# Kernel tuning notes

Measured on AMD Instinct MI355X. Metric: run time of the kernel, lower is better.

## Reference

```python
import jax, jax.numpy as jnp
import numpy as np

B, T, NE, NH, HD = 4, 1024, 768, 12, 64
CURV = 0.0
EPS = 1e-6
LN_EPS = 1e-5
ROPE_BASE = 10000.0


def project(x, k):
    # Lift Euclidean vector onto Lorentz hyperboloid with curvature K = exp(k):
    # time coord t = sqrt(K + ||x||^2) so that <lx, lx>_L = -K.
    K = jnp.exp(k)
    t = jnp.sqrt(K + jnp.sum(x * x, axis=-1, keepdims=True))
    return jnp.concatenate([t, x], axis=-1)


def lorentz_distance(lq, lk, k):
    # lq, lk: (B, H, T, D+1); k: (1, H, 1, 1) log-curvature.
    # d = sqrt(K) * arccosh(clamp(-<q,k>_L / K, 1+eps))
    K = jnp.exp(k)
    inner = (jnp.einsum('bhid,bhjd->bhij', lq[..., 1:], lk[..., 1:])
             - jnp.einsum('bhi,bhj->bhij', lq[..., 0], lk[..., 0]))
    c = jnp.clip(-inner / K, 1.0 + EPS, None)
    return jnp.sqrt(K) * jnp.arccosh(c)


def lorentz_norm(x):
    # sqrt(|<x,x>_L|) with <x,x>_L = -x0^2 + ||xs||^2  (keepdim)
    inner = -x[..., 0:1] ** 2 + jnp.sum(x[..., 1:] ** 2, axis=-1, keepdims=True)
    return jnp.sqrt(jnp.clip(-inner, EPS, None))


def rotary_tables():
    inv_freq = 1.0 / (ROPE_BASE ** (np.arange(0, HD, 2, dtype=np.float32) / HD))
    t = np.arange(T, dtype=np.float32)
    freqs = np.outer(t, inv_freq)  # (T, HD/2)
    cos = jnp.asarray(np.cos(freqs))[None, :, None, :]  # (1,T,1,HD/2)
    sin = jnp.asarray(np.sin(freqs))[None, :, None, :]
    return cos, sin


def apply_rotary(x, cos, sin):
    # x: (B, T, H, HD)
    x1, x2 = x[..., : HD // 2], x[..., HD // 2:]
    return jnp.concatenate([x1 * cos + x2 * sin, -x1 * sin + x2 * cos], axis=-1)


def layernorm(y, g, b):
    m = jnp.mean(y, axis=-1, keepdims=True)
    v = jnp.mean((y - m) ** 2, axis=-1, keepdims=True)
    return (y - m) / jnp.sqrt(v + LN_EPS) * g + b


def setup_inputs() -> dict:
    key = jax.random.key(0)
    ks = jax.random.split(key, 8)
    s = 0.02
    return {
        'x': jax.random.normal(ks[0], (B, T, NE), dtype=jnp.float32),
        'block_curvature': jnp.asarray(CURV, dtype=jnp.float32),
        'mlp_curvature': jnp.asarray(CURV, dtype=jnp.float32),
        'attn_curvatures': jnp.ones((1, NH, 1, 1), dtype=jnp.float32) * CURV,
        'qkv_w': jax.random.normal(ks[1], (3 * NE, NE + 1), dtype=jnp.float32) * s,
        'attn_proj_w': jax.random.normal(ks[2], (NE, (HD + 1) * NH), dtype=jnp.float32) * s,
        'attn_proj_b': jnp.zeros((NE,), dtype=jnp.float32),
        'mlp_expand_w': jax.random.normal(ks[3], (4 * NE + 3, NE + 1), dtype=jnp.float32) * s,
        'mlp_expand_b': jnp.zeros((4 * NE + 3,), dtype=jnp.float32),
        'mlp_shrink_w': jax.random.normal(ks[4], (NE, 4 * (NE + 1)), dtype=jnp.float32) * s,
        'mlp_shrink_b': jnp.zeros((NE,), dtype=jnp.float32),
        'ln_g': jnp.ones((NE,), dtype=jnp.float32),
        'ln_b': jnp.zeros((NE,), dtype=jnp.float32),
    }


def reference(x, block_curvature, mlp_curvature, attn_curvatures, qkv_w,
              attn_proj_w, attn_proj_b, mlp_expand_w, mlp_expand_b,
              mlp_shrink_w, mlp_shrink_b, ln_g, ln_b):
    cos, sin = rotary_tables()
    causal_bias = jnp.where(
        jnp.triu(jnp.ones((T, T), dtype=bool), k=1), -jnp.inf, 0.0).astype(jnp.float32)

    def block_norm(lx):
        return project(layernorm(lx[..., 1:], ln_g, ln_b), block_curvature)

    def attn(lx):
        qkv = lx @ qkv_w.T  # (B, T, 3*NE)
        q, k, v = jnp.split(qkv, 3, axis=-1)
        q = apply_rotary(q.reshape(B, T, NH, HD), cos, sin)
        k = apply_rotary(k.reshape(B, T, NH, HD), cos, sin)
        v = v.reshape(B, T, NH, HD)
        lq = project(q.transpose(0, 2, 1, 3), attn_curvatures)  # (B,H,T,HD+1)
        lk = project(k.transpose(0, 2, 1, 3), attn_curvatures)
        lv = project(v.transpose(0, 2, 1, 3), attn_curvatures)
        dis = lorentz_distance(lq, lk, attn_curvatures)  # (B,H,T,T)
        aw = jax.nn.softmax(-dis + causal_bias, axis=-1)
        a = jnp.einsum('bhij,bhjd->bhid', aw, lv)  # (B,H,T,HD+1)
        a = a * jnp.sqrt(jnp.exp(attn_curvatures)) / lorentz_norm(a)
        a = a.transpose(0, 2, 1, 3).reshape(B, T, NH * (HD + 1))
        a = a @ attn_proj_w.T + attn_proj_b
        return project(a, block_curvature)

    def mlp(lx):
        h = lx @ mlp_expand_w.T + mlp_expand_b  # (B,T,4*NE+3)
        h = project(h, mlp_curvature)[..., 1:]  # drop time coord back to 4*NE+3
        h = jax.nn.gelu(h, approximate=False)
        h = project(h, mlp_curvature)  # (B,T,4*(NE+1))
        h = h @ mlp_shrink_w.T + mlp_shrink_b
        return project(h, block_curvature)

    def skip(lx, f_lx):
        return project(lx[..., 1:] + f_lx[..., 1:], block_curvature)

    lx = project(x, block_curvature)  # (B,T,NE+1)
    lx = skip(lx, attn(block_norm(lx)))
    lx = skip(lx, mlp(block_norm(lx)))
    return lx
```

## Files before the change

### kernel.cpp

```cpp
#include <hip/hip_runtime.h>
#include <cmath>

typedef unsigned short ushort_t;
typedef __attribute__((ext_vector_type(8))) short short8;
typedef __attribute__((ext_vector_type(4))) float floatx4;

#define NH    12
#define T     1024
#define ROWS  4096
#define NE    768
#define KPA   832
#define KPB   3136
#define NEXP  3200
#define HEXP  3075
#define NSPLIT 3

__device__ __forceinline__ ushort_t f2bf(float f) {
  union { float f; unsigned u; } v; v.f = f;
  unsigned r = v.u + 0x7fffu + ((v.u >> 16) & 1u);
  return (ushort_t)(r >> 16);
}
__device__ __forceinline__ ushort_t f2bf_trunc(float f) {
  union { float f; unsigned u; } v; v.f = f;
  return (ushort_t)(v.u >> 16);
}
__device__ __forceinline__ float bf2f(ushort_t b) {
  union { unsigned u; float f; } v; v.u = ((unsigned)b) << 16;
  return v.f;
}
__device__ __forceinline__ float blk_reduce_sum(float v, float* sm) {
  #pragma unroll
  for (int o = 32; o > 0; o >>= 1) v += __shfl_xor(v, o, 64);
  int lane = threadIdx.x & 63, w = threadIdx.x >> 6;
  __syncthreads();
  if (lane == 0) sm[w] = v;
  __syncthreads();
  return sm[0] + sm[1] + sm[2] + sm[3];
}
__device__ __forceinline__ float red16_sum(float v) {
  #pragma unroll
  for (int o = 1; o < 16; o <<= 1) v += __shfl_xor(v, o, 64);
  return v;
}

#define NB_A 7488
#define NB_B 2496
#define NB_C 10400
#define NB_D 9408
#define NB_E 16
__device__ __forceinline__ void cvt_elem(ushort_t* __restrict__ dst,
                                         const float* __restrict__ src,
                                         int idx, int srcRows, int srcK, int dstK) {
  int r = idx / dstK, c = idx - r * dstK;
  dst[idx] = (r < srcRows && c < srcK) ? f2bf(src[(size_t)r * srcK + c]) : (ushort_t)0;
}
__global__ __launch_bounds__(256) void prep_kernel(
    ushort_t* __restrict__ qkv_wb, const float* __restrict__ qkvw,
    ushort_t* __restrict__ proj_wb, const float* __restrict__ projw,
    ushort_t* __restrict__ exp_wb, const float* __restrict__ expw,
    ushort_t* __restrict__ shr_wb, const float* __restrict__ shrw,
    ushort_t* __restrict__ aout_bf,
    const float* __restrict__ xin, const float* __restrict__ g,
    const float* __restrict__ bb, const float* __restrict__ curv,
    ushort_t* __restrict__ lnp) {
  __shared__ float sm[4];
  int blk = blockIdx.x;
  int tid = threadIdx.x;
  if (blk < NB_A) {
    cvt_elem(qkv_wb, qkvw, blk * 256 + tid, 2304, 769, KPA);
  } else if (blk < NB_A + NB_B) {
    cvt_elem(proj_wb, projw, (blk - NB_A) * 256 + tid, 768, 780, KPA);
  } else if (blk < NB_A + NB_B + NB_C) {
    cvt_elem(exp_wb, expw, (blk - NB_A - NB_B) * 256 + tid, HEXP, 769, KPA);
  } else if (blk < NB_A + NB_B + NB_C + NB_D) {
    cvt_elem(shr_wb, shrw, (blk - NB_A - NB_B - NB_C) * 256 + tid, 768, 3076, KPB);
  } else if (blk < NB_A + NB_B + NB_C + NB_D + NB_E) {
    int r = (blk - NB_A - NB_B - NB_C - NB_D) * 256 + tid;
    ushort_t* p = aout_bf + (size_t)r * KPA + 780;
    #pragma unroll
    for (int j = 0; j < KPA - 780; ++j) p[j] = 0;
  } else {
    const int row = blk - (NB_A + NB_B + NB_C + NB_D + NB_E);
    const float* xr = xin + (size_t)row * NE;
    float xv[3];
    float s = 0.f, ss = 0.f;
    #pragma unroll
    for (int i = 0; i < 3; ++i) {
      xv[i] = xr[tid + 256 * i];
      s += xv[i]; ss += xv[i] * xv[i];
    }
    s = blk_reduce_sum(s, sm);
    ss = blk_reduce_sum(ss, sm);
    float mean = s * (1.f / 768.f);
    float var = ss * (1.f / 768.f) - mean * mean;
    float rstd = rsqrtf(var + 1e-5f);
    float yv[3]; float ys = 0.f;
    #pragma unroll
    for (int i = 0; i < 3; ++i) {
      int c = tid + 256 * i;
      yv[i] = (xv[i] - mean) * rstd * g[c] + bb[c];
      ys += yv[i] * yv[i];
    }
    ys = blk_reduce_sum(ys, sm);
    float tc = sqrtf(expf(curv[0]) + ys);
    ushort_t* orow = lnp + (size_t)row * KPA;
    #pragma unroll
    for (int i = 0; i < 3; ++i) orow[1 + tid + 256 * i] = f2bf(yv[i]);
    if (tid == 0) orow[0] = f2bf(tc);
    if (tid < KPA - 769) orow[769 + tid] = 0;
  }
}

__global__ __launch_bounds__(256) void gemm_bf16(
    const ushort_t* __restrict__ A, int lda,
    const ushort_t* __restrict__ W, int ldw,
    void* __restrict__ Cout, int ldc,
    int nkTot, int cpt,
    const float* __restrict__ bias, int biasN,
    const float* __restrict__ res, int ldres,
    int outMode, void* __restrict__ Cp) {
  __shared__ ushort_t As[128 * 64];
  __shared__ ushort_t Bs[128 * 64];
  const int tid = threadIdx.x;
  const int w = tid >> 6, lane = tid & 63;

  int bx = blockIdx.x, by = blockIdx.y;
  {
    const int gx = gridDim.x, gy = gridDim.y;
    const int nwg = gx * gy;
    if ((nwg & 7) == 0) {
      int lin = by * gx + bx;
      int swz = (lin & 7) * (nwg >> 3) + (lin >> 3);
      bx = swz % gx;
      by = swz / gx;
    }
  }
  const int rowBase = by << 7;
  const int colBase = bx << 7;
  const int wm = (w & 1) * 64, wn = (w >> 1) * 64;
  const int lm = lane & 15, quad = lane >> 4;
  const int p0 = quad ^ (lm & 7);

  floatx4 acc[4][4];
  #pragma unroll
  for (int i = 0; i < 4; ++i)
    #pragma unroll
    for (int j = 0; j < 4; ++j) {
      floatx4 z = {0.f, 0.f, 0.f, 0.f};
      acc[i][j] = z;
    }

  const int kt0 = (int)blockIdx.z * cpt;
  const int kt1 = min(nkTot, kt0 + cpt);
  for (int kt = kt0; kt < kt1; ++kt) {
    __syncthreads();
    #pragma unroll
    for (int j = 0; j < 4; ++j) {
      int ci = j * 256 + tid;
      int r = ci >> 3;
      int g = (ci & 7) ^ (r & 7);
      const ushort_t* ga = A + (size_t)(rowBase + r) * lda + kt * 64 + g * 8;
      const ushort_t* gb = W + (size_t)(colBase + r) * ldw + kt * 64 + g * 8;
      __builtin_amdgcn_global_load_lds(
          (const __attribute__((address_space(1))) void*)ga,
          (__attribute__((address_space(3))) void*)&As[(j * 256 + w * 64) * 8],
          16, 0, 0);
      __builtin_amdgcn_global_load_lds(
          (const __attribute__((address_space(1))) void*)gb,
          (__attribute__((address_space(3))) void*)&Bs[(j * 256 + w * 64) * 8],
          16, 0, 0);
    }
    __syncthreads();

    #pragma unroll
    for (int s = 0; s < 2; ++s) {
      const int ps = s ? (p0 ^ 4) : p0;
      short8 af[4], bfr[4];
      #pragma unroll
      for (int i = 0; i < 4; ++i) {
        af[i]  = *(const short8*)&As[(wm + i * 16 + lm) * 64 + ps * 8];
        bfr[i] = *(const short8*)&Bs[(wn + i * 16 + lm) * 64 + ps * 8];
      }
      #pragma unroll
      for (int i = 0; i < 4; ++i)
        #pragma unroll
        for (int jn = 0; jn < 4; ++jn)
          acc[i][jn] = __builtin_amdgcn_mfma_f32_16x16x32_bf16(
              af[i], bfr[jn], acc[i][jn], 0, 0, 0);
    }
  }

  if (gridDim.z > 1) {
    ushort_t* dst = (ushort_t*)Cp + (size_t)blockIdx.z * ROWS * ldc;
    #pragma unroll
    for (int i = 0; i < 4; ++i)
      #pragma unroll
      for (int jn = 0; jn < 4; ++jn) {
        const int col = colBase + wn + jn * 16 + lm;
        #pragma unroll
        for (int rg = 0; rg < 4; ++rg) {
          const int row = rowBase + wm + i * 16 + quad * 4 + rg;
          dst[(size_t)row * ldc + col] = f2bf(acc[i][jn][rg]);
        }
      }
  } else if (outMode == 1) {
    ushort_t* C = (ushort_t*)Cout;
    #pragma unroll
    for (int i = 0; i < 4; ++i)
      #pragma unroll
      for (int jn = 0; jn < 4; ++jn) {
        const int col = colBase + wn + jn * 16 + lm;
        const float bv = bias ? ((col < biasN) ? bias[col] : 0.f) : 0.f;
        #pragma unroll
        for (int rg = 0; rg < 4; ++rg) {
          const int row = rowBase + wm + i * 16 + quad * 4 + rg;
          C[(size_t)row * ldc + col] = f2bf(acc[i][jn][rg] + bv);
        }
      }
  } else {
    float* C = (float*)Cout;
    #pragma unroll
    for (int i = 0; i < 4; ++i)
      #pragma unroll
      for (int jn = 0; jn < 4; ++jn) {
        const int col = colBase + wn + jn * 16 + lm;
        const float bv = bias ? ((col < biasN) ? bias[col] : 0.f) : 0.f;
        #pragma unroll
        for (int rg = 0; rg < 4; ++rg) {
          const int row = rowBase + wm + i * 16 + quad * 4 + rg;
          float o = acc[i][jn][rg] + bv;
          if (res) o += res[(size_t)row * ldres + col];
          C[(size_t)row * ldc + col] = o;
        }
      }
  }
}

__global__ __launch_bounds__(256) void rope_project(
    const ushort_t* __restrict__ qkvp, const float* __restrict__ ac,
    ushort_t* __restrict__ qb, ushort_t* __restrict__ kb, ushort_t* __restrict__ vtb,
    float* __restrict__ q0, float* __restrict__ k0, float* __restrict__ v0) {
  int gid = blockIdx.x * 4 + (threadIdx.x >> 6);
  int lane = threadIdx.x & 63;
  int h = gid % NH;
  int bt = gid / NH;
  int t = bt & (T - 1);
  int b = bt >> 10;
  size_t base = (size_t)bt * 2304 + h * 64;
  const ushort_t* p1 = qkvp + (size_t)ROWS * 2304;
  float qv = bf2f(qkvp[base + lane])        + bf2f(p1[base + lane]);
  float kv = bf2f(qkvp[base + 768 + lane])  + bf2f(p1[base + 768 + lane]);
  float vv = bf2f(qkvp[base + 1536 + lane]) + bf2f(p1[base + 1536 + lane]);
  int f = lane & 31;
  float ang = (float)t * __builtin_amdgcn_exp2f(-(float)f * 0.4152410118661534f);
  float sn, cs;
  sincosf(ang, &sn, &cs);
  float qp = __shfl(qv, lane ^ 32, 64);
  float kp = __shfl(kv, lane ^ 32, 64);
  float qr = (lane < 32) ? (qv * cs + qp * sn) : (-qp * sn + qv * cs);
  float kr = (lane < 32) ? (kv * cs + kp * sn) : (-kp * sn + kv * cs);
  float Kh = expf(ac[h]);
  float sq = qr * qr, sk = kr * kr, sv = vv * vv;
  #pragma unroll
  for (int o = 32; o > 0; o >>= 1) {
    sq += __shfl_xor(sq, o, 64);
    sk += __shfl_xor(sk, o, 64);
    sv += __shfl_xor(sv, o, 64);
  }
  size_t idx = ((size_t)(b * NH + h) * T + t);
  qb[idx * 64 + lane] = f2bf(qr);
  kb[idx * 64 + lane] = f2bf(kr);
  vtb[(size_t)(b * NH + h) * (64 * T) + (size_t)lane * T + t] = f2bf(vv);
  if (lane == 0) {
    q0[idx] = sqrtf(Kh + sq);
    k0[idx] = sqrtf(Kh + sk);
    v0[idx] = sqrtf(Kh + sv);
  }
}

__global__ __launch_bounds__(512, 4) void attn_kernel(
    const ushort_t* __restrict__ qb, const ushort_t* __restrict__ kb,
    const ushort_t* __restrict__ vtb,
    const float* __restrict__ q0, const float* __restrict__ k0,
    const float* __restrict__ v0,
    const float* __restrict__ ac,
    ushort_t* __restrict__ Opart, float* __restrict__ lpart,
    float* __restrict__ a0part) {
  __shared__ ushort_t QP[8 * 1152];
  __shared__ ushort_t Ks[2][64 * 64];
  __shared__ ushort_t Vts[2][64 * 64];

  int sIdx, qtile, bh;
  {
    const int lin = ((int)blockIdx.z * (int)gridDim.y + (int)blockIdx.y) * (int)gridDim.x
                    + (int)blockIdx.x;
    const int c = lin & 7;
    const int r = lin >> 3;
    bh = c + 8 * (r / 24);
    const int t24 = r % 24;
    sIdx = t24 % NSPLIT;
    qtile = (T / 128) - 1 - (t24 / NSPLIT);
  }
  const int h = bh % NH;
  const int qt0 = qtile * 128;
  const int tid = threadIdx.x;
  const int w = tid >> 6, lane = tid & 63;
  const int lm = lane & 15, quad = lane >> 4;
  const int wm = w * 16;
  const int sw = lm & 7;
  const int preg = w * 1152;

  const int n = 2 * qtile + 2;
  const int kbeg = (n * sIdx) / NSPLIT;
  const int kend = (n * (sIdx + 1)) / NSPLIT;
  const size_t pb = (size_t)(sIdx * 48 + bh) * T;

  if (kbeg >= kend) {
    #pragma unroll
    for (int r = 0; r < 4; ++r) {
      const int i = qt0 + wm + quad * 4 + r;
      ushort_t* orow = Opart + (pb + i) * 64;
      #pragma unroll
      for (int nt = 0; nt < 4; ++nt) orow[nt * 16 + lm] = 0;
      if (lm == 0) { lpart[pb + i] = 0.f; a0part[pb + i] = 0.f; }
    }
    return;
  }

  const float Kh = expf(ac[h]);
  const float sqrtK = sqrtf(Kh);
  const float invK = 1.0f / Kh;
  const float nsK = -sqrtK;
  const bool k1 = (Kh == 1.0f);

  {
    const ushort_t* qtp = qb + ((size_t)bh * T + qt0) * 64;
    #pragma unroll
    for (int j = 0; j < 2; ++j) {
      int g = j * 8 + w;
      int ci = g * 64 + lane;
      int r = ci >> 3;
      int clog = ((ci & 7) ^ (r & 7)) * 8;
      __builtin_amdgcn_global_load_lds(
          (const __attribute__((address_space(1))) void*)(qtp + r * 64 + clog),
          (__attribute__((address_space(3))) void*)&QP[(g >> 1) * 1152 + (g & 1) * 512],
          16, 0, 0);
    }
  }
  const ushort_t* kbase = kb + (size_t)bh * T * 64;
  const ushort_t* vbh = vtb + (size_t)bh * (64 * T);
  const float* k0row = k0 + (size_t)bh * T;
  const float* v0row = v0 + (size_t)bh * T;
  const int ldr = tid >> 3;
  const int ldcs = ((tid & 7) ^ (ldr & 7)) * 8;
  {
    const int j0 = kbeg * 64;
    __builtin_amdgcn_global_load_lds(
        (const __attribute__((address_space(1))) void*)(kbase + (size_t)(j0 + ldr) * 64 + ldcs),
        (__attribute__((address_space(3))) void*)&Ks[0][w * 512], 16, 0, 0);
    __builtin_amdgcn_global_load_lds(
        (const __attribute__((address_space(1))) void*)(vbh + (size_t)ldr * T + j0 + ldcs),
        (__attribute__((address_space(3))) void*)&Vts[0][w * 512], 16, 0, 0);
  }
  float k0n[4], v0n[4];
  #pragma unroll
  for (int jt = 0; jt < 4; ++jt) {
    k0n[jt] = k0row[kbeg * 64 + jt * 16 + lm];
    v0n[jt] = v0row[kbeg * 64 + jt * 16 + lm];
  }
  float q0rv[4];
  #pragma unroll
  for (int r = 0; r < 4; ++r)
    q0rv[r] = q0[(size_t)bh * T + qt0 + wm + quad * 4 + r];

  asm volatile("s_waitcnt vmcnt(0)" ::: "memory");
  __builtin_amdgcn_s_barrier();
  __builtin_amdgcn_sched_barrier(0);

  short8 qf0 = *(const short8*)&QP[preg + lm * 64 + ((0 + quad) ^ sw) * 8];
  short8 qf1 = *(const short8*)&QP[preg + lm * 64 + ((4 + quad) ^ sw) * 8];
  asm volatile("" : "+v"(qf0), "+v"(qf1));

  float lsum[4], a0r[4];
  floatx4 oacc[4];
  #pragma unroll
  for (int r = 0; r < 4; ++r) { lsum[r] = 0.f; a0r[r] = 0.f; }
  #pragma unroll
  for (int nt = 0; nt < 4; ++nt) { floatx4 z = {0.f,0.f,0.f,0.f}; oacc[nt] = z; }

  int cur = 0;
  for (int kt = kbeg; kt < kend; ++kt) {
    const bool hasNext = (kt + 1 < kend);
    float k0i[4], v0v[4];
    #pragma unroll
    for (int jt = 0; jt < 4; ++jt) { k0i[jt] = k0n[jt] * invK; v0v[jt] = v0n[jt]; }

    if (hasNext) {
      const int j0n = (kt + 1) * 64;
      __builtin_amdgcn_global_load_lds(
          (const __attribute__((address_space(1))) void*)(kbase + (size_t)(j0n + ldr) * 64 + ldcs),
          (__attribute__((address_space(3))) void*)&Ks[cur ^ 1][w * 512], 16, 0, 0);
      __builtin_amdgcn_global_load_lds(
          (const __attribute__((address_space(1))) void*)(vbh + (size_t)ldr * T + j0n + ldcs),
          (__attribute__((address_space(3))) void*)&Vts[cur ^ 1][w * 512], 16, 0, 0);
      #pragma unroll
      for (int jt = 0; jt < 4; ++jt) {
        k0n[jt] = k0row[j0n + jt * 16 + lm];
        v0n[jt] = v0row[j0n + jt * 16 + lm];
      }
    }

    const int j0 = kt * 64;
    const ushort_t* Kc = Ks[cur];
    const ushort_t* Vc = Vts[cur];

    floatx4 sacc[4];
    __builtin_amdgcn_s_setprio(1);
    #pragma unroll
    for (int jt = 0; jt < 4; ++jt) {
      const int krow = jt * 16 + lm;
      short8 kf0 = *(const short8*)&Kc[krow * 64 + ((0 + quad) ^ sw) * 8];
      short8 kf1 = *(const short8*)&Kc[krow * 64 + ((4 + quad) ^ sw) * 8];
      floatx4 z = {0.f, 0.f, 0.f, 0.f};
      z = __builtin_amdgcn_mfma_f32_16x16x32_bf16(qf0, kf0, z, 0, 0, 0);
      z = __builtin_amdgcn_mfma_f32_16x16x32_bf16(qf1, kf1, z, 0, 0, 0);
      sacc[jt] = z;
    }
    __builtin_amdgcn_s_setprio(0);

    const bool maskT = (kt >= 2 * qtile);
    if (k1) {
      #pragma unroll
      for (int r = 0; r < 4; ++r) {
        const int i = qt0 + wm + quad * 4 + r;
        float ls = 0.f, a0s = 0.f;
        #pragma unroll
        for (int jt = 0; jt < 4; ++jt) {
          float c = fmaf(-invK, sacc[jt][r], q0rv[r] * k0i[jt]);
          c = fmaxf(c, 1.000001f);
          float p = c - sqrtf(fmaf(c, c, -1.f));
          if (maskT && (j0 + jt * 16 + lm > i)) p = 0.f;
          ushort_t pb2 = f2bf_trunc(p);
          QP[preg + (quad * 4 + r) * 72 + jt * 16 + lm] = pb2;
          float pf = bf2f(pb2);
          ls += pf;
          a0s = fmaf(pf, v0v[jt], a0s);
        }
        lsum[r] += ls;
        a0r[r] += a0s;
      }
    } else {
      #pragma unroll
      for (int r = 0; r < 4; ++r) {
        const int i = qt0 + wm + quad * 4 + r;
        float ls = 0.f, a0s = 0.f;
        #pragma unroll
        for (int jt = 0; jt < 4; ++jt) {
          float c = fmaf(-invK, sacc[jt][r], q0rv[r] * k0i[jt]);
          c = fmaxf(c, 1.000001f);
          float z = c + sqrtf(fmaf(c, c, -1.f));
          float p = __builtin_amdgcn_exp2f(nsK * __builtin_amdgcn_logf(z));
          if (maskT && (j0 + jt * 16 + lm > i)) p = 0.f;
          ushort_t pb2 = f2bf_trunc(p);
          QP[preg + (quad * 4 + r) * 72 + jt * 16 + lm] = pb2;
          float pf = bf2f(pb2);
          ls += pf;
          a0s = fmaf(pf, v0v[jt], a0s);
        }
        lsum[r] += ls;
        a0r[r] += a0s;
      }
    }

    short8 pf0 = *(const short8*)&QP[preg + lm * 72 + quad * 8];
    short8 pf1 = *(const short8*)&QP[preg + lm * 72 + 32 + quad * 8];
    __builtin_amdgcn_s_setprio(1);
    #pragma unroll
    for (int nt = 0; nt < 4; ++nt) {
      const int vrow = nt * 16 + lm;
      short8 vf0 = *(const short8*)&Vc[vrow * 64 + ((0 + quad) ^ sw) * 8];
      short8 vf1 = *(const short8*)&Vc[vrow * 64 + ((4 + quad) ^ sw) * 8];
      oacc[nt] = __builtin_amdgcn_mfma_f32_16x16x32_bf16(pf0, vf0, oacc[nt], 0, 0, 0);
      oacc[nt] = __builtin_amdgcn_mfma_f32_16x16x32_bf16(pf1, vf1, oacc[nt], 0, 0, 0);
    }
    __builtin_amdgcn_s_setprio(0);

    if (hasNext) {
      asm volatile("s_waitcnt vmcnt(0)" ::: "memory");
      __builtin_amdgcn_s_barrier();
      __builtin_amdgcn_sched_barrier(0);
    }
    cur ^= 1;
  }

  #pragma unroll
  for (int r = 0; r < 4; ++r) {
    float lf = red16_sum(lsum[r]);
    float a0f = red16_sum(a0r[r]);
    const int i = qt0 + wm + quad * 4 + r;
    ushort_t* orow = Opart + (pb + i) * 64;
    #pragma unroll
    for (int nt = 0; nt < 4; ++nt) orow[nt * 16 + lm] = f2bf(oacc[nt][r]);
    if (lm == 0) { lpart[pb + i] = lf; a0part[pb + i] = a0f; }
  }
}

__global__ __launch_bounds__(256) void attn_combine(
    const ushort_t* __restrict__ Opart, const float* __restrict__ lpart,
    const float* __restrict__ a0part,
    const float* __restrict__ ac, ushort_t* __restrict__ aout) {
  const int widx = blockIdx.x * 4 + (threadIdx.x >> 6);
  const int lane = threadIdx.x & 63;
  const int bh = widx >> 10;
  const int t = widx & 1023;
  const int h = bh % NH, b = bh / NH;
  float L = 0.f, A0 = 0.f, O = 0.f;
  #pragma unroll
  for (int sp = 0; sp < NSPLIT; ++sp) {
    const size_t r = (size_t)(sp * 48 + bh) * T + t;
    L += lpart[r];
    A0 += a0part[r];
    O += bf2f(Opart[r * 64 + lane]);
  }
  const float invl = 1.f / L;
  float av = O * invl;
  float ssq = av * av;
  #pragma unroll
  for (int o = 32; o > 0; o >>= 1) ssq += __shfl_xor(ssq, o, 64);
  float a0n = A0 * invl;
  float nsq = fmaxf(a0n * a0n - ssq, 1e-6f);
  float Kh = expf(ac[h]);
  float scale = sqrtf(Kh) * rsqrtf(nsq);
  ushort_t* orow = aout + (size_t)(b * T + t) * KPA + h * 65;
  orow[1 + lane] = f2bf(av * scale);
  if (lane == 0) orow[0] = f2bf(a0n * scale);
}

__global__ __launch_bounds__(256) void gelu_project(
    const ushort_t* __restrict__ hsrc, const float* __restrict__ bias,
    const float* __restrict__ curv, ushort_t* __restrict__ hp) {
  __shared__ float sm[4];
  const int row = blockIdx.x;
  const int tid = threadIdx.x;
  const ushort_t* hr0 = hsrc + (size_t)row * NEXP;
  const ushort_t* hr1 = hr0 + (size_t)ROWS * NEXP;
  float gv[13];
  float ss = 0.f;
  #pragma unroll
  for (int i = 0; i < 13; ++i) {
    int c = tid + 256 * i;
    float xx = (c < HEXP) ? (bf2f(hr0[c]) + bf2f(hr1[c]) + bias[c]) : 0.f;
    float gg = 0.5f * xx * (1.f + erff(xx * 0.70710678118654752f));
    gv[i] = gg; ss += gg * gg;
  }
  ss = blk_reduce_sum(ss, sm);
  float tc = sqrtf(expf(curv[0]) + ss);
  ushort_t* orow = hp + (size_t)row * KPB;
  #pragma unroll
  for (int i = 0; i < 13; ++i) {
    int c = tid + 256 * i;
    if (c < HEXP) orow[1 + c] = f2bf(gv[i]);
  }
  if (tid == 0) orow[0] = f2bf(tc);
  if (tid < KPB - (HEXP + 1)) orow[HEXP + 1 + tid] = 0;
}

__global__ __launch_bounds__(256) void reduce_ln_project(
    const ushort_t* __restrict__ Cp, int nsplit,
    const float* __restrict__ bias, const float* __restrict__ res,
    float* __restrict__ x2out,
    const float* __restrict__ g, const float* __restrict__ bb,
    const float* __restrict__ curv, ushort_t* __restrict__ lnp) {
  __shared__ float sm[4];
  const int row = blockIdx.x;
  const int tid = threadIdx.x;
  float xv[3];
  float s = 0.f, ss = 0.f;
  #pragma unroll
  for (int i = 0; i < 3; ++i) {
    const int c = tid + 256 * i;
    float v = bias[c] + res[(size_t)row * NE + c];
    for (int sp = 0; sp < nsplit; ++sp)
      v += bf2f(Cp[(size_t)sp * ROWS * NE + (size_t)row * NE + c]);
    x2out[(size_t)row * NE + c] = v;
    xv[i] = v;
    s += v; ss += v * v;
  }
  s = blk_reduce_sum(s, sm);
  ss = blk_reduce_sum(ss, sm);
  float mean = s * (1.f / 768.f);
  float var = ss * (1.f / 768.f) - mean * mean;
  float rstd = rsqrtf(var + 1e-5f);
  float yv[3]; float ys = 0.f;
  #pragma unroll
  for (int i = 0; i < 3; ++i) {
    int c = tid + 256 * i;
    yv[i] = (xv[i] - mean) * rstd * g[c] + bb[c];
    ys += yv[i] * yv[i];
  }
  ys = blk_reduce_sum(ys, sm);
  float tc = sqrtf(expf(curv[0]) + ys);
  ushort_t* orow = lnp + (size_t)row * KPA;
  #pragma unroll
  for (int i = 0; i < 3; ++i) orow[1 + tid + 256 * i] = f2bf(yv[i]);
  if (tid == 0) orow[0] = f2bf(tc);
  if (tid < KPA - 769) orow[769 + tid] = 0;
}

__global__ __launch_bounds__(256) void reduce_final_project(
    const ushort_t* __restrict__ Cp, int nsplit,
    const float* __restrict__ bias, const float* __restrict__ res,
    const float* __restrict__ curv, float* __restrict__ out) {
  __shared__ float sm[4];
  const int row = blockIdx.x;
  const int tid = threadIdx.x;
  float v[3]; float ss = 0.f;
  #pragma unroll
  for (int i = 0; i < 3; ++i) {
    const int c = tid + 256 * i;
    float t = bias[c] + res[(size_t)row * NE + c];
    for (int sp = 0; sp < nsplit; ++sp)
      t += bf2f(Cp[(size_t)sp * ROWS * NE + (size_t)row * NE + c]);
    v[i] = t; ss += t * t;
  }
  ss = blk_reduce_sum(ss, sm);
  float tc = sqrtf(expf(curv[0]) + ss);
  float* o = out + (size_t)row * 769;
  #pragma unroll
  for (int i = 0; i < 3; ++i) o[1 + tid + 256 * i] = v[i];
  if (tid == 0) o[0] = tc;
}

extern "C" void kernel_launch(void* const* d_in, const int* in_sizes, int n_in,
                              void* d_out, int out_size, void* d_ws, size_t ws_size,
                              hipStream_t stream) {
  (void)in_sizes; (void)n_in; (void)out_size; (void)ws_size;
  const float* x     = (const float*)d_in[0];
  const float* bc    = (const float*)d_in[1];
  const float* mc    = (const float*)d_in[2];
  const float* ac    = (const float*)d_in[3];
  const float* qkvw  = (const float*)d_in[4];
  const float* projw = (const float*)d_in[5];
  const float* projb = (const float*)d_in[6];
  const float* expw  = (const float*)d_in[7];
  const float* expb  = (const float*)d_in[8];
  const float* shrw  = (const float*)d_in[9];
  const float* shrb  = (const float*)d_in[10];
  const float* lng   = (const float*)d_in[11];
  const float* lnb   = (const float*)d_in[12];
  float* out = (float*)d_out;

  float* x2 = (float*)d_ws;
  ushort_t* qkv_wb  = (ushort_t*)(x2 + (size_t)ROWS * NE);
  ushort_t* proj_wb = qkv_wb + (size_t)2304 * KPA;
  ushort_t* exp_wb  = proj_wb + (size_t)768 * KPA;
  ushort_t* shr_wb  = exp_wb + (size_t)NEXP * KPA;
  ushort_t* lnp_bf  = shr_wb + (size_t)768 * KPB;
  ushort_t* aout_bf = lnp_bf + (size_t)ROWS * KPA;
  char* r2 = (char*)(aout_bf + (size_t)ROWS * KPA);
  ushort_t* qkvp = (ushort_t*)r2;
  ushort_t* qbb = qkvp + (size_t)2 * ROWS * 2304;
  ushort_t* kbb = qbb + (size_t)48 * T * 64;
  ushort_t* vtb = kbb + (size_t)48 * T * 64;
  float* q0b = (float*)(vtb + (size_t)48 * T * 64);
  float* k0b = q0b + (size_t)48 * T;
  float* v0b = k0b + (size_t)48 * T;
  ushort_t* Opart = (ushort_t*)(v0b + (size_t)48 * T);
  float* lpart = (float*)(Opart + (size_t)NSPLIT * 48 * T * 64);
  float* a0part = lpart + (size_t)NSPLIT * 48 * T;
  ushort_t* ppartP = (ushort_t*)r2;
  ushort_t* hbbf = (ushort_t*)r2;
  ushort_t* hp_bf = hbbf + (size_t)2 * ROWS * NEXP;
  ushort_t* ppartS = (ushort_t*)r2;

  prep_kernel<<<NB_A + NB_B + NB_C + NB_D + NB_E + ROWS, 256, 0, stream>>>(
      qkv_wb, qkvw, proj_wb, projw, exp_wb, expw, shr_wb, shrw, aout_bf,
      x, lng, lnb, bc, lnp_bf);
  gemm_bf16<<<dim3(2304 / 128, ROWS / 128, 2), 256, 0, stream>>>(
      lnp_bf, KPA, qkv_wb, KPA, nullptr, 2304, KPA / 64, 7,
      nullptr, 0, nullptr, 0, 0, qkvp);
  rope_project<<<(ROWS * NH) / 4, 256, 0, stream>>>(qkvp, ac, qbb, kbb, vtb, q0b, k0b, v0b);
  attn_kernel<<<dim3(NSPLIT, T / 128, 48), 512, 0, stream>>>(
      qbb, kbb, vtb, q0b, k0b, v0b, ac, Opart, lpart, a0part);
  attn_combine<<<(48 * T) / 4, 256, 0, stream>>>(Opart, lpart, a0part, ac, aout_bf);
  gemm_bf16<<<dim3(768 / 128, ROWS / 128, 2), 256, 0, stream>>>(
      aout_bf, KPA, proj_wb, KPA, nullptr, NE, KPA / 64, 7,
      nullptr, 0, nullptr, 0, 0, ppartP);
  reduce_ln_project<<<ROWS, 256, 0, stream>>>(
      ppartP, 2, projb, x, x2, lng, lnb, bc, lnp_bf);
  gemm_bf16<<<dim3(NEXP / 128, ROWS / 128, 2), 256, 0, stream>>>(
      lnp_bf, KPA, exp_wb, KPA, nullptr, NEXP, KPA / 64, 7,
      nullptr, 0, nullptr, 0, 0, hbbf);
  gelu_project<<<ROWS, 256, 0, stream>>>(hbbf, expb, mc, hp_bf);
  gemm_bf16<<<dim3(768 / 128, ROWS / 128, 4), 256, 0, stream>>>(
      hp_bf, KPB, shr_wb, KPB, nullptr, NE, KPB / 64, 13,
      nullptr, 0, nullptr, 0, 0, ppartS);
  reduce_final_project<<<ROWS, 256, 0, stream>>>(
      ppartS, 4, shrb, x2, bc, out);
}
```

Baseline: 359.2 us.

## Double-buffer GEMM LDS tiles with BK=32 to overlap loads and MFMA

The bf16 GEMM K-tile shrinks from 64 to 32 and uses two LDS buffers. The next tile is prefetched with global_load_lds while MFMAs run on the current one, which replaces the two barriers per iteration with one wait-and-barrier. The swizzle is adapted to the 32-wide rows, and the launch k-tile counts and per-split chunk sizes are updated to match. The risk is that each barrier now covers half as much MFMA work, so per-iteration overhead rises.

```diff
diff --git a/kernel.cpp b/kernel.cpp
--- a/kernel.cpp
+++ b/kernel.cpp
@@ -119,8 +119,8 @@
     const float* __restrict__ bias, int biasN,
     const float* __restrict__ res, int ldres,
     int outMode, void* __restrict__ Cp) {
-  __shared__ ushort_t As[128 * 64];
-  __shared__ ushort_t Bs[128 * 64];
+  __shared__ ushort_t As[2][128 * 32];
+  __shared__ ushort_t Bs[2][128 * 32];
   const int tid = threadIdx.x;
   const int w = tid >> 6, lane = tid & 63;
 
@@ -139,7 +139,7 @@
   const int colBase = bx << 7;
   const int wm = (w & 1) * 64, wn = (w >> 1) * 64;
   const int lm = lane & 15, quad = lane >> 4;
-  const int p0 = quad ^ (lm & 7);
+  const int fr = quad ^ ((lm >> 1) & 3);
 
   floatx4 acc[4][4];
   #pragma unroll
@@ -152,42 +152,55 @@
 
   const int kt0 = (int)blockIdx.z * cpt;
   const int kt1 = min(nkTot, kt0 + cpt);
-  for (int kt = kt0; kt < kt1; ++kt) {
-    __syncthreads();
-    #pragma unroll
-    for (int j = 0; j < 4; ++j) {
-      int ci = j * 256 + tid;
-      int r = ci >> 3;
-      int g = (ci & 7) ^ (r & 7);
-      const ushort_t* ga = A + (size_t)(rowBase + r) * lda + kt * 64 + g * 8;
-      const ushort_t* gb = W + (size_t)(colBase + r) * ldw + kt * 64 + g * 8;
+
+  auto stage = [&](int kt, int bsel) {
+    #pragma unroll
+    for (int j = 0; j < 2; ++j) {
+      int slot = j * 256 + tid;
+      int r = slot >> 2;
+      int c = (slot & 3) ^ ((r >> 1) & 3);
+      const ushort_t* ga = A + (size_t)(rowBase + r) * lda + kt * 32 + c * 8;
+      const ushort_t* gb = W + (size_t)(colBase + r) * ldw + kt * 32 + c * 8;
       __builtin_amdgcn_global_load_lds(
           (const __attribute__((address_space(1))) void*)ga,
-          (__attribute__((address_space(3))) void*)&As[(j * 256 + w * 64) * 8],
+          (__attribute__((address_space(3))) void*)&As[bsel][(j * 256 + w * 64) * 8],
           16, 0, 0);
       __builtin_amdgcn_global_load_lds(
           (const __attribute__((address_space(1))) void*)gb,
-          (__attribute__((address_space(3))) void*)&Bs[(j * 256 + w * 64) * 8],
+          (__attribute__((address_space(3))) void*)&Bs[bsel][(j * 256 + w * 64) * 8],
           16, 0, 0);
     }
-    __syncthreads();
-
-    #pragma unroll
-    for (int s = 0; s < 2; ++s) {
-      const int ps = s ? (p0 ^ 4) : p0;
-      short8 af[4], bfr[4];
+  };
+
+  stage(kt0, 0);
+  asm volatile("s_waitcnt vmcnt(0)" ::: "memory");
+  __builtin_amdgcn_s_barrier();
+  __builtin_amdgcn_sched_barrier(0);
+
+  int cur = 0;
+  for (int kt = kt0; kt < kt1; ++kt) {
+    const bool hasNext = (kt + 1 < kt1);
+    if (hasNext) stage(kt + 1, cur ^ 1);
+
+    short8 af[4], bfr[4];
+    #pragma unroll
+    for (int i = 0; i < 4; ++i) {
+      af[i]  = *(const short8*)&As[cur][(wm + i * 16 + lm) * 32 + fr * 8];
+      bfr[i] = *(const short8*)&Bs[cur][(wn + i * 16 + lm) * 32 + fr * 8];
+    }
+    #pragma unroll
+    for (int i = 0; i < 4; ++i)
       #pragma unroll
-      for (int i = 0; i < 4; ++i) {
-        af[i]  = *(const short8*)&As[(wm + i * 16 + lm) * 64 + ps * 8];
-        bfr[i] = *(const short8*)&Bs[(wn + i * 16 + lm) * 64 + ps * 8];
-      }
-      #pragma unroll
-      for (int i = 0; i < 4; ++i)
-        #pragma unroll
-        for (int jn = 0; jn < 4; ++jn)
-          acc[i][jn] = __builtin_amdgcn_mfma_f32_16x16x32_bf16(
-              af[i], bfr[jn], acc[i][jn], 0, 0, 0);
-    }
+      for (int jn = 0; jn < 4; ++jn)
+        acc[i][jn] = __builtin_amdgcn_mfma_f32_16x16x32_bf16(
+            af[i], bfr[jn], acc[i][jn], 0, 0, 0);
+
+    if (hasNext) {
+      asm volatile("s_waitcnt vmcnt(0)" ::: "memory");
+      __builtin_amdgcn_s_barrier();
+      __builtin_amdgcn_sched_barrier(0);
+    }
+    cur ^= 1;
   }
 
   if (gridDim.z > 1) {
@@ -677,23 +690,23 @@
       qkv_wb, qkvw, proj_wb, projw, exp_wb, expw, shr_wb, shrw, aout_bf,
       x, lng, lnb, bc, lnp_bf);
   gemm_bf16<<<dim3(2304 / 128, ROWS / 128, 2), 256, 0, stream>>>(
-      lnp_bf, KPA, qkv_wb, KPA, nullptr, 2304, KPA / 64, 7,
+      lnp_bf, KPA, qkv_wb, KPA, nullptr, 2304, KPA / 32, 13,
       nullptr, 0, nullptr, 0, 0, qkvp);
   rope_project<<<(ROWS * NH) / 4, 256, 0, stream>>>(qkvp, ac, qbb, kbb, vtb, q0b, k0b, v0b);
   attn_kernel<<<dim3(NSPLIT, T / 128, 48), 512, 0, stream>>>(
       qbb, kbb, vtb, q0b, k0b, v0b, ac, Opart, lpart, a0part);
   attn_combine<<<(48 * T) / 4, 256, 0, stream>>>(Opart, lpart, a0part, ac, aout_bf);
   gemm_bf16<<<dim3(768 / 128, ROWS / 128, 2), 256, 0, stream>>>(
-      aout_bf, KPA, proj_wb, KPA, nullptr, NE, KPA / 64, 7,
+      aout_bf, KPA, proj_wb, KPA, nullptr, NE, KPA / 32, 13,
       nullptr, 0, nullptr, 0, 0, ppartP);
   reduce_ln_project<<<ROWS, 256, 0, stream>>>(
       ppartP, 2, projb, x, x2, lng, lnb, bc, lnp_bf);
   gemm_bf16<<<dim3(NEXP / 128, ROWS / 128, 2), 256, 0, stream>>>(
-      lnp_bf, KPA, exp_wb, KPA, nullptr, NEXP, KPA / 64, 7,
+      lnp_bf, KPA, exp_wb, KPA, nullptr, NEXP, KPA / 32, 13,
       nullptr, 0, nullptr, 0, 0, hbbf);
   gelu_project<<<ROWS, 256, 0, stream>>>(hbbf, expb, mc, hp_bf);
   gemm_bf16<<<dim3(768 / 128, ROWS / 128, 4), 256, 0, stream>>>(
-      hp_bf, KPB, shr_wb, KPB, nullptr, NE, KPB / 64, 13,
+      hp_bf, KPB, shr_wb, KPB, nullptr, NE, KPB / 32, 25,
       nullptr, 0, nullptr, 0, 0, ppartS);
   reduce_final_project<<<ROWS, 256, 0, stream>>>(
       ppartS, 4, shrb, x2, bc, out);
```

Measured after the change: 409.8 us. +14.1%, slower.
